# Performance work log

Measured on AMD Instinct MI355X. Metric: run time of the kernel, lower is better.

The kernel has to match this reference:

```python
import jax, jax.numpy as jnp
import numpy as np

N_NODES = 100000


def gcn_conv(x, edge_index, W, b, n):
    """PyG-style GCNConv: h = D^-1/2 (A + I) D^-1/2 (x W) + b."""
    h = x @ W  # [n, out]
    loops = jnp.arange(n, dtype=edge_index.dtype)
    src = jnp.concatenate([edge_index[0], loops])
    dst = jnp.concatenate([edge_index[1], loops])
    deg = jax.ops.segment_sum(jnp.ones_like(dst, dtype=h.dtype), dst, num_segments=n)
    dinv = jnp.where(deg > 0, jax.lax.rsqrt(deg), 0.0)
    norm = dinv[src] * dinv[dst]  # [E+n]
    msg = h[src] * norm[:, None]
    out = jax.ops.segment_sum(msg, dst, num_segments=n)
    return out + b


def setup_inputs() -> dict:
    key = jax.random.key(0)
    ks = jax.random.split(key, 12)
    n, f, hid, c, e = N_NODES, 128, 16, 32, 3200000
    x = jax.random.normal(ks[0], (n, f), dtype=jnp.float32)
    edge_index_pos = jax.random.randint(ks[1], (2, e), 0, n, dtype=jnp.int32)
    edge_index_neg = jax.random.randint(ks[2], (2, e), 0, n, dtype=jnp.int32)
    def glorot(k, fi, fo):
        lim = np.sqrt(6.0 / (fi + fo)).astype(np.float32)
        return jax.random.uniform(k, (fi, fo), minval=-lim, maxval=lim, dtype=jnp.float32)
    return {
        "x": x,
        "edge_index_pos": edge_index_pos,
        "edge_index_neg": edge_index_neg,
        "W1p": glorot(ks[3], f, hid), "b1p": jnp.zeros((hid,), jnp.float32),
        "W1n": glorot(ks[4], f, hid), "b1n": jnp.zeros((hid,), jnp.float32),
        "W2p": glorot(ks[5], hid, c), "b2p": jnp.zeros((c,), jnp.float32),
        "W2n": glorot(ks[6], hid, c), "b2n": jnp.zeros((c,), jnp.float32),
    }


def reference(x, edge_index_pos, edge_index_neg, W1p, b1p, W1n, b1n, W2p, b2p, W2n, b2n):
    n = x.shape[0]
    # layer 1: relu(pos) - relu(neg)
    h = (jax.nn.relu(gcn_conv(x, edge_index_pos, W1p, b1p, n))
         - jax.nn.relu(gcn_conv(x, edge_index_neg, W1n, b1n, n)))
    # dropout is identity in eval mode (training=False)
    h = (jax.nn.relu(gcn_conv(h, edge_index_pos, W2p, b2p, n))
         - jax.nn.relu(gcn_conv(h, edge_index_neg, W2n, b2n, n)))
    return jax.nn.log_softmax(h, axis=1)
```

## Files before the change

### kernel.cpp

```cpp
#include <hip/hip_runtime.h>
#include <hip/hip_fp16.h>


#define BSHIFT 8
#define BSZ 256
#define MAX_NBK 512
#define FILL_CAP 13056
#define SORT_CAP 12032

typedef int   i32x4 __attribute__((ext_vector_type(4)));

__device__ __forceinline__ int chunk_of_block(int bid, int NCH) {
  return (NCH % 8 == 0) ? (bid % 8) * (NCH / 8) + bid / 8 : bid;
}


__global__ __launch_bounds__(256) void bucket_count2(
    const int* __restrict__ eP, const int* __restrict__ eN,
    int E, int CH, int NCH, int NBK, int* __restrict__ ccP, int* __restrict__ ccN) {
  __shared__ int cnt[MAX_NBK];
  const int* dsts = (blockIdx.y ? eN : eP) + E;
  int* cc = blockIdx.y ? ccN : ccP;
  const int c = chunk_of_block(blockIdx.x, NCH);
  for (int i = threadIdx.x; i < NBK; i += 256) cnt[i] = 0;
  __syncthreads();
  int base = c * CH, end = min(E, base + CH);
  for (int idx = base + threadIdx.x * 4; idx < end; idx += 1024) {
    if (idx + 4 <= end) {
      i32x4 d = __builtin_nontemporal_load((const i32x4*)(dsts + idx));
      atomicAdd(&cnt[d.x >> BSHIFT], 1);
      atomicAdd(&cnt[d.y >> BSHIFT], 1);
      atomicAdd(&cnt[d.z >> BSHIFT], 1);
      atomicAdd(&cnt[d.w >> BSHIFT], 1);
    } else {
      for (int k = idx; k < end; ++k) atomicAdd(&cnt[dsts[k] >> BSHIFT], 1);
    }
  }
  __syncthreads();
  for (int i = threadIdx.x; i < NBK; i += 256)
    cc[(size_t)c * NBK + i] = cnt[i];
}

__global__ __launch_bounds__(512) void col_scan2(
    int* __restrict__ ccP, int* __restrict__ ccN, int NCH, int NBK,
    int* __restrict__ totP, int* __restrict__ totN) {
  __shared__ int s[512];
  int* cc = blockIdx.y ? ccN : ccP;
  int* tot = blockIdx.y ? totN : totP;
  int b = blockIdx.x, t = threadIdx.x;
  int v = (t < NCH) ? cc[(size_t)t * NBK + b] : 0;
  s[t] = v;
  for (int off = 1; off < 512; off <<= 1) {
    __syncthreads();
    int a = (t >= off) ? s[t - off] : 0;
    __syncthreads();
    s[t] += a;
  }
  __syncthreads();
  if (t < NCH) cc[(size_t)t * NBK + b] = s[t] - v;
  if (t == 511) tot[b] = s[511];
}

__global__ __launch_bounds__(512) void bucket_fill3(
    const int* __restrict__ eP, const int* __restrict__ eN,
    int E, int CH, int NCH, int NBK,
    const int* __restrict__ ccP, const int* __restrict__ ccN,
    const int* __restrict__ totP, const int* __restrict__ totN,
    unsigned* __restrict__ prP, unsigned* __restrict__ prN) {
  __shared__ unsigned obuf[FILL_CAP];
  __shared__ int chofs[MAX_NBK], hist[MAX_NBK], lofs[MAX_NBK], cur[MAX_NBK];
  __shared__ int bas_l[MAX_NBK];
  __shared__ int s[512];
  const int* edges = blockIdx.y ? eN : eP;
  const int* cc = blockIdx.y ? ccN : ccP;
  const int* tot = blockIdx.y ? totN : totP;
  unsigned* pairs = blockIdx.y ? prN : prP;
  const int c = chunk_of_block(blockIdx.x, NCH);
  const int t = threadIdx.x;

  int h = 0;
  if (t < NBK) {
    int o0 = cc[(size_t)c * NBK + t];
    int o1 = (c + 1 < NCH) ? cc[(size_t)(c + 1) * NBK + t] : tot[t];
    chofs[t] = o0;
    h = o1 - o0;
    hist[t] = h;
  }
  s[t] = h;
  for (int off = 1; off < 512; off <<= 1) {
    __syncthreads();
    int a = (t >= off) ? s[t - off] : 0;
    __syncthreads();
    s[t] += a;
  }
  __syncthreads();
  if (t < NBK) { lofs[t] = s[t] - hist[t]; cur[t] = s[t] - hist[t]; }
  __syncthreads();

  int tv = (t < NBK) ? tot[t] : 0;
  s[t] = tv;
  for (int off = 1; off < 512; off <<= 1) {
    __syncthreads();
    int a = (t >= off) ? s[t - off] : 0;
    __syncthreads();
    s[t] += a;
  }
  __syncthreads();
  if (t < NBK) bas_l[t] = s[t] - tv;
  __syncthreads();

  int base = c * CH, end = min(E, base + CH);
  for (int idx = base + t * 4; idx < end; idx += 2048) {
    if (idx + 4 <= end) {
      i32x4 sv = __builtin_nontemporal_load((const i32x4*)(edges + idx));
      i32x4 dv = __builtin_nontemporal_load((const i32x4*)(edges + E + idx));
      int p0 = atomicAdd(&cur[dv.x >> BSHIFT], 1);
      obuf[p0] = (unsigned)sv.x | ((unsigned)(dv.x & (BSZ - 1)) << 24);
      int p1 = atomicAdd(&cur[dv.y >> BSHIFT], 1);
      obuf[p1] = (unsigned)sv.y | ((unsigned)(dv.y & (BSZ - 1)) << 24);
      int p2 = atomicAdd(&cur[dv.z >> BSHIFT], 1);
      obuf[p2] = (unsigned)sv.z | ((unsigned)(dv.z & (BSZ - 1)) << 24);
      int p3 = atomicAdd(&cur[dv.w >> BSHIFT], 1);
      obuf[p3] = (unsigned)sv.w | ((unsigned)(dv.w & (BSZ - 1)) << 24);
    } else {
      for (int k = idx; k < end; ++k) {
        int sv = edges[k], d = edges[E + k];
        int pos = atomicAdd(&cur[d >> BSHIFT], 1);
        obuf[pos] = (unsigned)sv | ((unsigned)(d & (BSZ - 1)) << 24);
      }
    }
  }
  __syncthreads();

  const int wv = t >> 6, ln = t & 63;
  for (int b = wv; b < NBK; b += 8) {
    int cnt2 = hist[b], lo = lofs[b];
    unsigned* dst = pairs + (size_t)bas_l[b] + chofs[b];
    for (int j = ln; j < cnt2; j += 64) dst[j] = obuf[lo + j];
  }
}

__global__ __launch_bounds__(256) void tile_sort3(
    const unsigned* __restrict__ prP, const unsigned* __restrict__ prN,
    const int* __restrict__ totP, const int* __restrict__ totN, int n, int E,
    float* __restrict__ dinvP, float* __restrict__ dinvN,
    int* __restrict__ rowP, int* __restrict__ rowN,
    unsigned* __restrict__ srcsP, unsigned* __restrict__ srcsN) {
  __shared__ unsigned obuf[SORT_CAP];
  __shared__ int hist[BSZ];
  __shared__ int scn[BSZ];
  __shared__ int cur[BSZ];
  __shared__ int red[256];
  const unsigned* pairs = blockIdx.y ? prN : prP;
  const int* tot = blockIdx.y ? totN : totP;
  float* dinv = blockIdx.y ? dinvN : dinvP;
  int* rowoff = blockIdx.y ? rowN : rowP;
  unsigned* srcs = blockIdx.y ? srcsN : srcsP;
  const int b = blockIdx.x, t = threadIdx.x;

  int part = 0;
  for (int j = t; j < b; j += 256) part += tot[j];
  red[t] = part;
  __syncthreads();
  for (int off = 128; off > 0; off >>= 1) {
    if (t < off) red[t] += red[t + off];
    __syncthreads();
  }
  const int s0 = red[0];
  const int cnt = tot[b];
  const int s1 = s0 + cnt;
  if (b == (int)gridDim.x - 1 && t == 0) rowoff[n] = E;

  hist[t] = 0;
  __syncthreads();
  for (int i = s0 + t; i < s1; i += 256)
    atomicAdd(&hist[__builtin_nontemporal_load(pairs + i) >> 24], 1);
  __syncthreads();
  scn[t] = hist[t];
  __syncthreads();
  for (int off = 1; off < BSZ; off <<= 1) {
    int v = (t >= off) ? scn[t - off] : 0;
    __syncthreads();
    scn[t] += v;
    __syncthreads();
  }
  {
    int excl = scn[t] - hist[t];
    cur[t] = excl;
    int node = b * BSZ + t;
    if (node < n) {
      rowoff[node] = s0 + excl;
      dinv[node] = rsqrtf(1.0f + (float)hist[t]);
    }
  }
  __syncthreads();
  if (cnt <= SORT_CAP) {
    for (int i = s0 + t; i < s1; i += 256) {
      unsigned p = __builtin_nontemporal_load(pairs + i);
      int pos = atomicAdd(&cur[p >> 24], 1);
      obuf[pos] = p & 0xFFFFFFu;
    }
    __syncthreads();
    for (int i = t; i < cnt; i += 256) srcs[s0 + i] = obuf[i];
  } else {
    for (int i = s0 + t; i < s1; i += 256) {
      unsigned p = __builtin_nontemporal_load(pairs + i);
      int pos = atomicAdd(&cur[p >> 24], 1);
      srcs[s0 + pos] = p & 0xFFFFFFu;
    }
  }
}

__global__ __launch_bounds__(256) void xw1_kernel(
    const float* __restrict__ x, const float* __restrict__ Wp, const float* __restrict__ Wn,
    const float* __restrict__ dinvP, const float* __restrict__ dinvN,
    __half* __restrict__ hp, __half* __restrict__ hn, int n)
{
  __shared__ float xs[16 * 132];
  __shared__ float wp[128 * 16], wn[128 * 16];
  const int tid = threadIdx.x;
  const int rowBase = blockIdx.x * 16;

  for (int idx = tid; idx < 512; idx += 256) {
    ((float4*)wp)[idx] = ((const float4*)Wp)[idx];
    ((float4*)wn)[idx] = ((const float4*)Wn)[idx];
  }
  const int nrows = min(16, n - rowBase);
  for (int idx = tid; idx < nrows * 32; idx += 256) {
    int r = idx >> 5, c4 = idx & 31;
    float4 v = ((const float4*)(x + (size_t)(rowBase + r) * 128))[c4];
    *(float4*)(xs + r * 132 + c4 * 4) = v;
  }
  __syncthreads();

  const int r = tid >> 4, c = tid & 15;
  const int i = rowBase + r;
  if (i < n) {
    float ap = 0.f, an = 0.f;
    #pragma unroll
    for (int k = 0; k < 128; ++k) {
      float xv = xs[r * 132 + k];
      ap += xv * wp[k * 16 + c];
      an += xv * wn[k * 16 + c];
    }
    hp[(size_t)i * 16 + c] = __float2half(ap * dinvP[i]);
    hn[(size_t)i * 16 + c] = __float2half(an * dinvN[i]);
  }
}

__device__ __forceinline__ void fma_mix2(float& aLo, float& aHi, unsigned h2, float one) {
  asm("v_fma_mix_f32 %0, %2, %3, %0 op_sel:[0,0,0] op_sel_hi:[1,0,0]\n\t"
      "v_fma_mix_f32 %1, %2, %3, %1 op_sel:[1,0,0] op_sel_hi:[1,0,0]"
      : "+v"(aLo), "+v"(aHi)
      : "v"(h2), "v"(one));
}

__device__ __forceinline__ void seg_sum4(
    const unsigned* __restrict__ srcs, int e, int e1,
    const __half* __restrict__ tab, int lane4, float one,
    float& f0, float& f1, float& f2, float& f3)
{
  float g0 = 0.f, g1 = 0.f, g2 = 0.f, g3 = 0.f;
  for (; e + 8 <= e1; e += 8) {
    unsigned a[8];
    #pragma unroll
    for (int j = 0; j < 8; ++j) a[j] = srcs[e + j];
    uint2 v[8];
    #pragma unroll
    for (int j = 0; j < 8; ++j)
      v[j] = *(const uint2*)(tab + (size_t)a[j] * 16 + lane4 * 4);
    #pragma unroll
    for (int j = 0; j < 8; j += 2) {
      fma_mix2(f0, f1, v[j].x, one);
      fma_mix2(f2, f3, v[j].y, one);
      fma_mix2(g0, g1, v[j + 1].x, one);
      fma_mix2(g2, g3, v[j + 1].y, one);
    }
  }
  for (; e + 2 <= e1; e += 2) {
    unsigned a0 = srcs[e], a1 = srcs[e + 1];
    uint2 v0 = *(const uint2*)(tab + (size_t)a0 * 16 + lane4 * 4);
    uint2 v1 = *(const uint2*)(tab + (size_t)a1 * 16 + lane4 * 4);
    fma_mix2(f0, f1, v0.x, one);
    fma_mix2(f2, f3, v0.y, one);
    fma_mix2(g0, g1, v1.x, one);
    fma_mix2(g2, g3, v1.y, one);
  }
  if (e < e1) {
    uint2 v = *(const uint2*)(tab + (size_t)srcs[e] * 16 + lane4 * 4);
    fma_mix2(f0, f1, v.x, one);
    fma_mix2(f2, f3, v.y, one);
  }
  f0 += g0; f1 += g1; f2 += g2; f3 += g3;
}

__global__ __launch_bounds__(256) void agg_split(
    const unsigned* __restrict__ srcP, const int* __restrict__ rowP,
    const unsigned* __restrict__ srcN, const int* __restrict__ rowN,
    const __half* __restrict__ inP, const __half* __restrict__ inN,
    const float* __restrict__ dinvP, const float* __restrict__ dinvN,
    float* __restrict__ tmpP, float* __restrict__ tmpN, int n)
{
  const int gb = blockIdx.x;
  const int xcd = gb & 7;
  const int sign = xcd >> 2;
  const int nblk = (gb >> 3) * 4 + (xcd & 3);
  const int lane4 = threadIdx.x & 3, grp = threadIdx.x >> 2;
  const int i = nblk * 64 + grp;
  if (i >= n) return;

  const unsigned* __restrict__ srcs = sign ? srcN : srcP;
  const int* __restrict__ row = sign ? rowN : rowP;
  const __half* __restrict__ tab = sign ? inN : inP;
  const float* __restrict__ dinv = sign ? dinvN : dinvP;
  float* __restrict__ tmp = sign ? tmpN : tmpP;

  const float one = 1.0f;
  float f0 = 0.f, f1 = 0.f, f2 = 0.f, f3 = 0.f;
  uint2 self = *(const uint2*)(tab + (size_t)i * 16 + lane4 * 4);
  fma_mix2(f0, f1, self.x, one);
  fma_mix2(f2, f3, self.y, one);
  seg_sum4(srcs, row[i], row[i + 1], tab, lane4, one, f0, f1, f2, f3);
  const float d = dinv[i];
  float4 o;
  o.x = f0 * d; o.y = f1 * d; o.z = f2 * d; o.w = f3 * d;
  *(float4*)(tmp + (size_t)i * 16 + lane4 * 4) = o;
}

__global__ __launch_bounds__(256) void combine1(
    const float* __restrict__ tmpP, const float* __restrict__ tmpN,
    const float* __restrict__ bp, const float* __restrict__ bn,
    const float* __restrict__ dinvP, const float* __restrict__ dinvN,
    __half* __restrict__ Gp, __half* __restrict__ Gn, int nq)
{
  int q = blockIdx.x * 256 + threadIdx.x;
  if (q >= nq) return;
  int i = q >> 2;
  float4 tp = ((const float4*)tmpP)[q];
  float4 tn = ((const float4*)tmpN)[q];
  float4 bpv = ((const float4*)bp)[q & 3];
  float4 bnv = ((const float4*)bn)[q & 3];
  float dp = dinvP[i], dn = dinvN[i];
  float h0 = fmaxf(bpv.x + tp.x, 0.f) - fmaxf(bnv.x + tn.x, 0.f);
  float h1 = fmaxf(bpv.y + tp.y, 0.f) - fmaxf(bnv.y + tn.y, 0.f);
  float h2 = fmaxf(bpv.z + tp.z, 0.f) - fmaxf(bnv.z + tn.z, 0.f);
  float h3 = fmaxf(bpv.w + tp.w, 0.f) - fmaxf(bnv.w + tn.w, 0.f);
  union { uint2 u; __half2 h[2]; } a, b;
  a.h[0] = __floats2half2_rn(h0 * dp, h1 * dp);
  a.h[1] = __floats2half2_rn(h2 * dp, h3 * dp);
  b.h[0] = __floats2half2_rn(h0 * dn, h1 * dn);
  b.h[1] = __floats2half2_rn(h2 * dn, h3 * dn);
  ((uint2*)Gp)[q] = a.u;
  ((uint2*)Gn)[q] = b.u;
}

__global__ __launch_bounds__(256) void final2(
    const float* __restrict__ Up, const float* __restrict__ Un,
    const float* __restrict__ W2p, const float* __restrict__ W2n,
    const float* __restrict__ b2p, const float* __restrict__ b2n,
    float* __restrict__ out, int n)
{
  __shared__ float wp[16 * 32], wn[16 * 32];
  for (int i = threadIdx.x; i < 512; i += 256) { wp[i] = W2p[i]; wn[i] = W2n[i]; }
  __syncthreads();

  const int tid = threadIdx.x;
  const int lane = tid & 15, grp = tid >> 4;
  const int i = blockIdx.x * 16 + grp;
  if (i >= n) return;

  float tp = Up[(size_t)i * 16 + lane];
  float tn = Un[(size_t)i * 16 + lane];

  float ap0 = b2p[lane], ap1 = b2p[lane + 16];
  float an0 = b2n[lane], an1 = b2n[lane + 16];
  #pragma unroll
  for (int k = 0; k < 16; ++k) {
    float tpk = __shfl(tp, k, 16);
    float tnk = __shfl(tn, k, 16);
    ap0 += tpk * wp[k * 32 + lane];
    ap1 += tpk * wp[k * 32 + lane + 16];
    an0 += tnk * wn[k * 32 + lane];
    an1 += tnk * wn[k * 32 + lane + 16];
  }
  float v0 = fmaxf(ap0, 0.f) - fmaxf(an0, 0.f);
  float v1 = fmaxf(ap1, 0.f) - fmaxf(an1, 0.f);
  float m = fmaxf(v0, v1);
  #pragma unroll
  for (int off = 8; off > 0; off >>= 1) m = fmaxf(m, __shfl_xor(m, off, 16));
  float s = __expf(v0 - m) + __expf(v1 - m);
  #pragma unroll
  for (int off = 8; off > 0; off >>= 1) s += __shfl_xor(s, off, 16);
  float ls = __logf(s);
  out[(size_t)i * 32 + lane] = v0 - m - ls;
  out[(size_t)i * 32 + lane + 16] = v1 - m - ls;
}

extern "C" void kernel_launch(void* const* d_in, const int* in_sizes, int n_in,
                              void* d_out, int out_size, void* d_ws, size_t ws_size,
                              hipStream_t stream) {
  const float* x   = (const float*)d_in[0];
  const int*   eP  = (const int*)d_in[1];
  const int*   eN  = (const int*)d_in[2];
  const float* W1p = (const float*)d_in[3];
  const float* b1p = (const float*)d_in[4];
  const float* W1n = (const float*)d_in[5];
  const float* b1n = (const float*)d_in[6];
  const float* W2p = (const float*)d_in[7];
  const float* b2p = (const float*)d_in[8];
  const float* W2n = (const float*)d_in[9];
  const float* b2n = (const float*)d_in[10];
  float* out = (float*)d_out;

  const int HID = in_sizes[4];
  const int F   = in_sizes[3] / HID;
  const int n   = in_sizes[0] / F;
  const int E   = in_sizes[1] / 2;
  (void)out_size; (void)n_in; (void)ws_size;

  const int NBK = (n + BSZ - 1) >> BSHIFT;
  const int CH  = (((E + 255) / 256) + 255) & ~255;
  const int NCH = (E + CH - 1) / CH;

  char* p = (char*)d_ws;
  auto alloc = [&](size_t bytes) { char* r = p; p += (bytes + 255) & ~(size_t)255; return r; };

  int*      ccP   = (int*)alloc((size_t)NCH * NBK * 4);
  int*      ccN   = (int*)alloc((size_t)NCH * NBK * 4);
  int*      totP  = (int*)alloc((size_t)NBK * 4);
  int*      totN  = (int*)alloc((size_t)NBK * 4);
  unsigned* prP   = (unsigned*)alloc((size_t)E * 4);
  unsigned* prN   = (unsigned*)alloc((size_t)E * 4);
  unsigned* srcP  = (unsigned*)alloc((size_t)E * 4);
  unsigned* srcN  = (unsigned*)alloc((size_t)E * 4);
  int*      rowP  = (int*)alloc((size_t)(n + 1) * 4);
  int*      rowN  = (int*)alloc((size_t)(n + 1) * 4);
  float*    dinvP = (float*)alloc((size_t)n * 4);
  float*    dinvN = (float*)alloc((size_t)n * 4);
  __half*   hsP   = (__half*)alloc((size_t)n * 16 * 2);
  __half*   hsN   = (__half*)alloc((size_t)n * 16 * 2);
  __half*   Gp    = (__half*)alloc((size_t)n * 16 * 2);
  __half*   Gn    = (__half*)alloc((size_t)n * 16 * 2);
  float*    tmpP  = (float*)alloc((size_t)n * 16 * 4);
  float*    tmpN  = (float*)alloc((size_t)n * 16 * 4);

  hipLaunchKernelGGL(bucket_count2, dim3(NCH, 2), dim3(256), 0, stream,
                     eP, eN, E, CH, NCH, NBK, ccP, ccN);
  hipLaunchKernelGGL(col_scan2, dim3(NBK, 2), dim3(512), 0, stream,
                     ccP, ccN, NCH, NBK, totP, totN);
  hipLaunchKernelGGL(bucket_fill3, dim3(NCH, 2), dim3(512), 0, stream,
                     eP, eN, E, CH, NCH, NBK, ccP, ccN, totP, totN, prP, prN);
  hipLaunchKernelGGL(tile_sort3, dim3(NBK, 2), dim3(256), 0, stream,
                     prP, prN, totP, totN, n, E, dinvP, dinvN, rowP, rowN, srcP, srcN);

  const int NB16 = (n + 15) / 16;
  const int NB64 = (n + 63) / 64;
  const int NBS  = ((NB64 + 3) / 4) * 4;
  const int GRID = NBS * 2;

  hipLaunchKernelGGL(xw1_kernel, dim3(NB16), dim3(256), 0, stream,
                     x, W1p, W1n, dinvP, dinvN, hsP, hsN, n);
  hipLaunchKernelGGL(agg_split, dim3(GRID), dim3(256), 0, stream,
                     srcP, rowP, srcN, rowN, hsP, hsN, dinvP, dinvN, tmpP, tmpN, n);
  hipLaunchKernelGGL(combine1, dim3((n * 4 + 255) / 256), dim3(256), 0, stream,
                     tmpP, tmpN, b1p, b1n, dinvP, dinvN, Gp, Gn, n * 4);

  hipLaunchKernelGGL(agg_split, dim3(GRID), dim3(256), 0, stream,
                     srcP, rowP, srcN, rowN, Gp, Gn, dinvP, dinvN, tmpP, tmpN, n);
  hipLaunchKernelGGL(final2, dim3(NB16), dim3(256), 0, stream,
                     tmpP, tmpN, W2p, W2n, b2p, b2n, out, n);
}
```

Before: 238.8 us.

## Privatize shared-memory histograms and double chunk count for edge bucketing

The bucket count and tile sort histograms are split into 2 and 4 per-thread sub-copies to spread LDS atomic contention, and the copies are summed afterwards. Edge chunks are halved in size (about 512 chunks instead of 256), which shrinks the fill buffer and raises grid parallelism. The per-bucket copy-out now uses 32-lane groups instead of 64-lane waves to suit the smaller buckets. Costs are extra LDS zeroing and reduction, more per-chunk count rows for the column scan, and a smaller sort buffer capacity that may push more tiles onto the slow direct-write path.

```diff
diff --git a/kernel.cpp b/kernel.cpp
--- a/kernel.cpp
+++ b/kernel.cpp
@@ -5,8 +5,8 @@
 #define BSHIFT 8
 #define BSZ 256
 #define MAX_NBK 512
-#define FILL_CAP 13056
-#define SORT_CAP 12032
+#define FILL_CAP 6272
+#define SORT_CAP 10240
 
 typedef int   i32x4 __attribute__((ext_vector_type(4)));
 
@@ -18,27 +18,28 @@
 __global__ __launch_bounds__(256) void bucket_count2(
     const int* __restrict__ eP, const int* __restrict__ eN,
     int E, int CH, int NCH, int NBK, int* __restrict__ ccP, int* __restrict__ ccN) {
-  __shared__ int cnt[MAX_NBK];
+  __shared__ int cnt[MAX_NBK][2];
   const int* dsts = (blockIdx.y ? eN : eP) + E;
   int* cc = blockIdx.y ? ccN : ccP;
   const int c = chunk_of_block(blockIdx.x, NCH);
-  for (int i = threadIdx.x; i < NBK; i += 256) cnt[i] = 0;
-  __syncthreads();
+  for (int i = threadIdx.x; i < NBK * 2; i += 256) ((int*)cnt)[i] = 0;
+  __syncthreads();
+  const int sub = threadIdx.x & 1;
   int base = c * CH, end = min(E, base + CH);
   for (int idx = base + threadIdx.x * 4; idx < end; idx += 1024) {
     if (idx + 4 <= end) {
       i32x4 d = __builtin_nontemporal_load((const i32x4*)(dsts + idx));
-      atomicAdd(&cnt[d.x >> BSHIFT], 1);
-      atomicAdd(&cnt[d.y >> BSHIFT], 1);
-      atomicAdd(&cnt[d.z >> BSHIFT], 1);
-      atomicAdd(&cnt[d.w >> BSHIFT], 1);
+      atomicAdd(&cnt[d.x >> BSHIFT][sub], 1);
+      atomicAdd(&cnt[d.y >> BSHIFT][sub], 1);
+      atomicAdd(&cnt[d.z >> BSHIFT][sub], 1);
+      atomicAdd(&cnt[d.w >> BSHIFT][sub], 1);
     } else {
-      for (int k = idx; k < end; ++k) atomicAdd(&cnt[dsts[k] >> BSHIFT], 1);
+      for (int k = idx; k < end; ++k) atomicAdd(&cnt[dsts[k] >> BSHIFT][sub], 1);
     }
   }
   __syncthreads();
   for (int i = threadIdx.x; i < NBK; i += 256)
-    cc[(size_t)c * NBK + i] = cnt[i];
+    cc[(size_t)c * NBK + i] = cnt[i][0] + cnt[i][1];
 }
 
 __global__ __launch_bounds__(512) void col_scan2(
@@ -132,11 +133,11 @@
   }
   __syncthreads();
 
-  const int wv = t >> 6, ln = t & 63;
-  for (int b = wv; b < NBK; b += 8) {
+  const int wv = t >> 5, ln = t & 31;
+  for (int b = wv; b < NBK; b += 16) {
     int cnt2 = hist[b], lo = lofs[b];
     unsigned* dst = pairs + (size_t)bas_l[b] + chofs[b];
-    for (int j = ln; j < cnt2; j += 64) dst[j] = obuf[lo + j];
+    for (int j = ln; j < cnt2; j += 32) dst[j] = obuf[lo + j];
   }
 }
 
@@ -147,7 +148,7 @@
     int* __restrict__ rowP, int* __restrict__ rowN,
     unsigned* __restrict__ srcsP, unsigned* __restrict__ srcsN) {
   __shared__ unsigned obuf[SORT_CAP];
-  __shared__ int hist[BSZ];
+  __shared__ int hist4[BSZ][4];
   __shared__ int scn[BSZ];
   __shared__ int cur[BSZ];
   __shared__ int red[256];
@@ -161,6 +162,7 @@
   int part = 0;
   for (int j = t; j < b; j += 256) part += tot[j];
   red[t] = part;
+  for (int i = t; i < BSZ * 4; i += 256) ((int*)hist4)[i] = 0;
   __syncthreads();
   for (int off = 128; off > 0; off >>= 1) {
     if (t < off) red[t] += red[t + off];
@@ -171,12 +173,12 @@
   const int s1 = s0 + cnt;
   if (b == (int)gridDim.x - 1 && t == 0) rowoff[n] = E;
 
-  hist[t] = 0;
-  __syncthreads();
+  const int sub = t & 3;
   for (int i = s0 + t; i < s1; i += 256)
-    atomicAdd(&hist[__builtin_nontemporal_load(pairs + i) >> 24], 1);
-  __syncthreads();
-  scn[t] = hist[t];
+    atomicAdd(&hist4[pairs[i] >> 24][sub], 1);
+  __syncthreads();
+  const int h = hist4[t][0] + hist4[t][1] + hist4[t][2] + hist4[t][3];
+  scn[t] = h;
   __syncthreads();
   for (int off = 1; off < BSZ; off <<= 1) {
     int v = (t >= off) ? scn[t - off] : 0;
@@ -185,12 +187,12 @@
     __syncthreads();
   }
   {
-    int excl = scn[t] - hist[t];
+    int excl = scn[t] - h;
     cur[t] = excl;
     int node = b * BSZ + t;
     if (node < n) {
       rowoff[node] = s0 + excl;
-      dinv[node] = rsqrtf(1.0f + (float)hist[t]);
+      dinv[node] = rsqrtf(1.0f + (float)h);
     }
   }
   __syncthreads();
@@ -419,7 +421,7 @@
   (void)out_size; (void)n_in; (void)ws_size;
 
   const int NBK = (n + BSZ - 1) >> BSHIFT;
-  const int CH  = (((E + 255) / 256) + 255) & ~255;
+  const int CH  = (((E + 511) / 512) + 3) & ~3;
   const int NCH = (E + CH - 1) / CH;
 
   char* p = (char*)d_ws;
```

Measured after the change: 227.7 us (median of 2 runs). 4.6% less time.
